# Kernel optimization log

Measured on AMD Instinct MI355X. Metric: run time of the kernel, lower is better.

## Reference

```python
import jax, jax.numpy as jnp
import numpy as np

MARGIN = 0.0  # init kwarg margin=0


def setup_inputs() -> dict:
    key = jax.random.key(0)
    k1, k2 = jax.random.split(key)
    inputs = jax.random.normal(k1, (4096, 2048), dtype=jnp.float32)
    targets = jax.random.randint(k2, (4096,), 0, 64, dtype=jnp.int64)
    return {"inputs": inputs, "targets": targets}


def _last_true_index(cond):
    # cond: (n, n) bool. Original torch loop zeros leading True entries until one
    # remains -> keeps the LAST True index per row.
    n = cond.shape[1]
    return (n - 1) - jnp.argmax(cond[:, ::-1], axis=1)


def reference(inputs, targets):
    n = inputs.shape[0]
    INF = jnp.asarray(jnp.inf, dtype=inputs.dtype)

    # pairwise euclidean distances: ||xi||^2 + ||xj||^2 - 2 xi.xj, clamp, sqrt
    sq = jnp.sum(inputs * inputs, axis=1)
    dist = sq[:, None] + sq[None, :] - 2.0 * (inputs @ inputs.T)
    dist = jnp.sqrt(jnp.clip(dist, 1e-12))  # (n, n)

    same = targets[:, None] == targets[None, :]  # (n, n) same-label mask

    # hardest positive / hardest negative per row
    dist_ap = jnp.where(same, dist, -INF).max(axis=1)
    dist_an = jnp.where(same, INF, dist).min(axis=1)

    # tie-broken indices (last occurrence, matching the torch loop)
    p = _last_true_index((dist == dist_ap[:, None]) & same)      # hardest pos idx
    q = _last_true_index((dist == dist_an[:, None]) & (~same))   # hardest neg idx

    # an2 = dist(hardest_pos_i, hardest_neg_i)
    dist_an2 = dist[p, q]

    # maskc: labels differing from both anchor's label and hardest-negative's label
    lbl_q = targets[q]
    maskc = (targets[None, :] != targets[:, None]) & (targets[None, :] != lbl_q[:, None])

    dist_q = dist[q]  # (n, n): distance rows of the hardest negatives
    ok_min = jnp.where(maskc, dist_q, INF).min(axis=1)
    r = _last_true_index((dist_q == ok_min[:, None]) & maskc)

    dist_an3 = dist[jnp.arange(n), r]  # dist(anchor, third-class sample)
    dist_an4 = dist_q[jnp.arange(n), r]  # dist(hardest neg, third-class sample) == ok_min

    # MarginRankingLoss(margin, reduce=False) with y=1: relu(ap - an + margin)
    loss = jax.nn.relu(dist_ap - dist_an + MARGIN)
    loss3 = jnp.abs(dist_an - dist_an2)
    loss4 = jnp.abs(dist_an3 - dist_an4)
    return (loss + loss3 + loss4).sum() / n
```

## Files before the change

### kernel.cpp

```cpp
#include <hip/hip_runtime.h>
#include <hip/hip_bf16.h>
#include <cstdint>

#define N_DIM 4096
#define K_DIM 2048
#define NKT 32
#define QSCALE 24.0f
#define QINV (1.0f / 24.0f)

typedef float floatx4 __attribute__((ext_vector_type(4)));
typedef int intx4 __attribute__((ext_vector_type(4)));
typedef unsigned short ushort8 __attribute__((ext_vector_type(8)));
typedef unsigned long long ull;

__device__ __forceinline__ unsigned short f2bf(float f) {
    unsigned int u = __builtin_bit_cast(unsigned int, f);
    unsigned int r = (u + 0x7fffu + ((u >> 16) & 1u)) >> 16;
    return (unsigned short)r;
}

__device__ __forceinline__ float bf2f(unsigned short b) {
    return __uint_as_float(((unsigned)b) << 16);
}

__device__ __forceinline__ void gld_lds16(const void* g, void* l) {
    __builtin_amdgcn_global_load_lds(
        (const __attribute__((address_space(1))) unsigned int*)g,
        (__attribute__((address_space(3))) unsigned int*)l,
        16, 0, 0);
}

__global__ __launch_bounds__(256)
void prep_kernel(const float* __restrict__ X, char* __restrict__ Qt,
                 int* __restrict__ sqi) {
    const int row = blockIdx.x;
    const int tid = threadIdx.x;
    const float* xr = X + (size_t)row * K_DIM;
    floatx4 a = *(const floatx4*)(xr + tid * 8);
    floatx4 b = *(const floatx4*)(xr + tid * 8 + 4);
    int s = 0;
    unsigned lo = 0, hi = 0;
#pragma unroll
    for (int e = 0; e < 4; ++e) {
        int v = __float2int_rn(a[e] * QSCALE);
        v = min(127, max(-127, v));
        s += v * v;
        lo |= ((unsigned)(v & 0xff)) << (8 * e);
        int w = __float2int_rn(b[e] * QSCALE);
        w = min(127, max(-127, w));
        s += w * w;
        hi |= ((unsigned)(w & 0xff)) << (8 * e);
    }
    *(int2*)(Qt + ((size_t)(tid >> 1) * 4096 + row) * 16 + (tid & 1) * 8) =
        make_int2((int)lo, (int)hi);
#pragma unroll
    for (int off = 32; off; off >>= 1) s += __shfl_down(s, off);
    __shared__ int wsum[4];
    const int wave = tid >> 6, lane = tid & 63;
    if (lane == 0) wsum[wave] = s;
    __syncthreads();
    if (tid == 0) sqi[row] = wsum[0] + wsum[1] + wsum[2] + wsum[3];
}

#define BAR() __builtin_amdgcn_s_barrier()
#define PRIO1() __builtin_amdgcn_s_setprio(1)
#define PRIO0() __builtin_amdgcn_s_setprio(0)
#define VMCNT3() asm volatile("s_waitcnt vmcnt(3)" ::: "memory")
#define VMCNT0() asm volatile("s_waitcnt vmcnt(0)" ::: "memory")
#define KTB 262144
#define STG(KT, BB) { \
    gld_lds16(aSt + (size_t)(KT) * KTB,          lds + (BB) + widB); \
    gld_lds16(aSt + (size_t)(KT) * KTB + 131072, lds + (BB) + 8192 + widB); \
    gld_lds16(bSt + (size_t)(KT) * KTB,          lds + (BB) + 16384 + widB); }

__global__ __launch_bounds__(512, 4)
void gemm_dist(const char* __restrict__ Qt, const int* __restrict__ sqi,
               unsigned short* __restrict__ Db) {
    __shared__ char lds[73728];
    const int tid = threadIdx.x;
    const int wid = tid >> 6, lane = tid & 63;
    const int wr = wid >> 1, wc = wid & 1;
    const int fr = lane & 15, ksub = lane >> 4;
    const int widB = wid * 1024;

    int rA[4], rB[4];
#pragma unroll
    for (int m = 0; m < 4; ++m) rA[m] = (ksub * 256 + wr * 64 + m * 16 + fr) * 16;
#pragma unroll
    for (int n = 0; n < 4; ++n) rB[n] = 16384 + (ksub * 128 + wc * 64 + n * 16 + fr) * 16;

    const int xcd = blockIdx.x & 7, kk = blockIdx.x >> 3;
    const int bi = (kk >> 3) | ((xcd & 1) << 3);
    const int bj = (kk & 7) | ((xcd >> 1) << 3);
    const int rowC0 = bi * 256, colC0 = bj * 128;

    const char* aSt = Qt + ((size_t)(tid >> 8) * 4096 + rowC0 + (tid & 255)) * 16;
    const char* bSt = Qt + ((size_t)(tid >> 7) * 4096 + colC0 + (tid & 127)) * 16;

    intx4 acc[4][4];
#pragma unroll
    for (int a1 = 0; a1 < 4; ++a1)
#pragma unroll
    for (int a2 = 0; a2 < 4; ++a2) acc[a1][a2] = (intx4){0, 0, 0, 0};
    intx4 af[4], bfv[4];

    STG(0, 0);
    STG(1, 24576);
    VMCNT3();
    BAR();

    int cb = 0, sb = 49152;
    for (int t = 0; t < NKT; ++t) {
        if (t < NKT - 2) STG(t + 2, sb);
#pragma unroll
        for (int m = 0; m < 4; ++m) af[m] = *(const intx4*)(lds + cb + rA[m]);
#pragma unroll
        for (int n = 0; n < 4; ++n) bfv[n] = *(const intx4*)(lds + cb + rB[n]);
        PRIO1();
#pragma unroll
        for (int n = 0; n < 4; ++n)
#pragma unroll
        for (int m = 0; m < 4; ++m)
            acc[n][m] = __builtin_amdgcn_mfma_i32_16x16x64_i8(
                af[m], bfv[n], acc[n][m], 0, 0, 0);
        PRIO0();
        if (t < NKT - 2) { VMCNT3(); } else if (t == NKT - 2) { VMCNT0(); }
        BAR();
        cb += 24576; if (cb >= 73728) cb = 0;
        sb += 24576; if (sb >= 73728) sb = 0;
    }

#pragma unroll
    for (int n = 0; n < 4; ++n) {
        const int col = colC0 + wc * 64 + n * 16 + fr;
        const int sqc = sqi[col];
#pragma unroll
        for (int m = 0; m < 4; ++m) {
            const int row0 = rowC0 + wr * 64 + m * 16 + ksub * 4;
#pragma unroll
            for (int r = 0; r < 4; ++r) {
                const int v = sqi[row0 + r] + sqc - 2 * acc[n][m][r];
                const float d = (v > 0) ? sqrtf((float)v) * QINV : 1e-6f;
                Db[(size_t)(row0 + r) * N_DIM + col] = f2bf(d);
            }
        }
    }
}

__global__ __launch_bounds__(256)
void stats_loss(const unsigned short* __restrict__ Db, const int* __restrict__ tgt,
                float* __restrict__ lossArr) {
    const int i = blockIdx.x, tid = threadIdx.x;
    const int ti = tgt[i];
    const unsigned short* row = Db + (size_t)i * N_DIM;
    ull kmax = 0ULL, kmin = ~0ULL;
#pragma unroll
    for (int it = 0; it < 2; ++it) {
        const int j0 = (it * 256 + tid) * 8;
        ushort8 d = *(const ushort8*)(row + j0);
        intx4 ta = *(const intx4*)(tgt + j0);
        intx4 tb = *(const intx4*)(tgt + j0 + 4);
#pragma unroll
        for (int e = 0; e < 8; ++e) {
            const int j = j0 + e;
            const int tl = (e < 4) ? ta[e] : tb[e - 4];
            const ull db = (ull)d[e] << 32;
            if (tl == ti) { ull k = db | (unsigned)j;  if (k > kmax) kmax = k; }
            else          { ull k = db | (unsigned)~j; if (k < kmin) kmin = k; }
        }
    }
    __shared__ ull sM[256], sN[256];
    sM[tid] = kmax; sN[tid] = kmin;
    __syncthreads();
    for (int off = 128; off; off >>= 1) {
        if (tid < off) {
            if (sM[tid + off] > sM[tid]) sM[tid] = sM[tid + off];
            if (sN[tid + off] < sN[tid]) sN[tid] = sN[tid + off];
        }
        __syncthreads();
    }
    const ull km = sM[0], kn = sN[0];
    const float ap = bf2f((unsigned short)(km >> 32));
    const int p = (int)(unsigned)(km & 0xFFFFFFFFu);
    const float an = bf2f((unsigned short)(kn >> 32));
    const int q = (int)~(unsigned)(kn & 0xFFFFFFFFu);
    __syncthreads();

    const int lq = tgt[q];
    const unsigned short* rowq = Db + (size_t)q * N_DIM;
    ull kr = ~0ULL;
#pragma unroll
    for (int it = 0; it < 2; ++it) {
        const int j0 = (it * 256 + tid) * 8;
        ushort8 d = *(const ushort8*)(rowq + j0);
        intx4 ta = *(const intx4*)(tgt + j0);
        intx4 tb = *(const intx4*)(tgt + j0 + 4);
#pragma unroll
        for (int e = 0; e < 8; ++e) {
            const int j = j0 + e;
            const int tl = (e < 4) ? ta[e] : tb[e - 4];
            if (tl != ti && tl != lq) {
                ull k = ((ull)d[e] << 32) | (unsigned)~j;
                if (k < kr) kr = k;
            }
        }
    }
    sN[tid] = kr;
    __syncthreads();
    for (int off = 128; off; off >>= 1) {
        if (tid < off) { if (sN[tid + off] < sN[tid]) sN[tid] = sN[tid + off]; }
        __syncthreads();
    }
    if (tid == 0) {
        const ull kk = sN[0];
        const float okmin = bf2f((unsigned short)(kk >> 32));
        const int r = (int)~(unsigned)(kk & 0xFFFFFFFFu);
        const float an2 = bf2f(Db[(size_t)p * N_DIM + q]);
        const float an3 = bf2f(Db[(size_t)i * N_DIM + r]);
        lossArr[i] = fmaxf(ap - an, 0.f) + fabsf(an - an2) + fabsf(an3 - okmin);
    }
}

__global__ __launch_bounds__(256)
void finred(const float* __restrict__ lossArr, float* __restrict__ out) {
    const int tid = threadIdx.x;
    float s = 0.f;
    for (int j = tid; j < N_DIM; j += 256) s += lossArr[j];
#pragma unroll
    for (int off = 32; off; off >>= 1) s += __shfl_down(s, off);
    __shared__ float w[4];
    const int wave = tid >> 6, lane = tid & 63;
    if (lane == 0) w[wave] = s;
    __syncthreads();
    if (tid == 0) out[0] = (w[0] + w[1] + w[2] + w[3]) * (1.0f / (float)N_DIM);
}

extern "C" void kernel_launch(void* const* d_in, const int* in_sizes, int n_in,
                              void* d_out, int out_size, void* d_ws, size_t ws_size,
                              hipStream_t stream) {
    const float* X = (const float*)d_in[0];
    const int* tgt = (const int*)d_in[1];
    float* out = (float*)d_out;

    char* w = (char*)d_ws;
    char* Qt = w;
    unsigned short* Db = (unsigned short*)(w + ((size_t)16 << 20));
    int* sqi = (int*)(w + ((size_t)80 << 20));
    float* lossArr = (float*)(sqi + N_DIM);

    prep_kernel<<<N_DIM, 256, 0, stream>>>(X, Qt, sqi);
    gemm_dist<<<512, 512, 0, stream>>>(Qt, sqi, Db);
    stats_loss<<<N_DIM, 256, 0, stream>>>(Db, tgt, lossArr);
    finred<<<1, 256, 0, stream>>>(lossArr, out);
}
```

Baseline: 78.61 us.

## Load A fragments directly into registers, stage only B through LDS

The A operand fragments now go straight from global memory into registers with inline-asm dwordx4 loads, double-buffered across two register sets. Only the B tile is still staged through LDS, using a smaller three-slot ring. This removes A's LDS write and read traffic and cuts LDS use from 72KB to 24KB per block. In exchange it raises register pressure, depends on hand-set vmcnt counts and sched_barriers for correctness, and uses less-coalesced global reads for A.

```diff
diff --git a/kernel.cpp b/kernel.cpp
--- a/kernel.cpp
+++ b/kernel.cpp
@@ -62,72 +62,75 @@
     if (tid == 0) sqi[row] = wsum[0] + wsum[1] + wsum[2] + wsum[3];
 }
 
-#define BAR() __builtin_amdgcn_s_barrier()
+#define BAR() { __builtin_amdgcn_s_barrier(); asm volatile("" ::: "memory"); }
 #define PRIO1() __builtin_amdgcn_s_setprio(1)
 #define PRIO0() __builtin_amdgcn_s_setprio(0)
-#define VMCNT3() asm volatile("s_waitcnt vmcnt(3)" ::: "memory")
-#define VMCNT0() asm volatile("s_waitcnt vmcnt(0)" ::: "memory")
+#define VMCNT5() { asm volatile("s_waitcnt vmcnt(5)" ::: "memory"); \
+                   __builtin_amdgcn_sched_barrier(0); }
+#define VMCNT0() { asm volatile("s_waitcnt vmcnt(0)" ::: "memory"); \
+                   __builtin_amdgcn_sched_barrier(0); }
 #define KTB 262144
-#define STG(KT, BB) { \
-    gld_lds16(aSt + (size_t)(KT) * KTB,          lds + (BB) + widB); \
-    gld_lds16(aSt + (size_t)(KT) * KTB + 131072, lds + (BB) + 8192 + widB); \
-    gld_lds16(bSt + (size_t)(KT) * KTB,          lds + (BB) + 16384 + widB); }
+#define LOAD_A(DST) { \
+    asm volatile("global_load_dwordx4 %0, %1, off"            : "=&v"(DST[0]) : "v"(aAddr)); \
+    asm volatile("global_load_dwordx4 %0, %1, off offset:256" : "=&v"(DST[1]) : "v"(aAddr)); \
+    asm volatile("global_load_dwordx4 %0, %1, off offset:512" : "=&v"(DST[2]) : "v"(aAddr)); \
+    asm volatile("global_load_dwordx4 %0, %1, off offset:768" : "=&v"(DST[3]) : "v"(aAddr)); \
+    aAddr += KTB; }
+#define MM16(AF) { _Pragma("unroll") for (int n_ = 0; n_ < 4; ++n_) { \
+    _Pragma("unroll") for (int m_ = 0; m_ < 4; ++m_) { \
+        acc[n_][m_] = __builtin_amdgcn_mfma_i32_16x16x64_i8( \
+            AF[m_], bfv[n_], acc[n_][m_], 0, 0, 0); } } }
+#define TILE_BODY(T, LD, USE) { \
+    if ((T) < NKT - 1) LOAD_A(LD); \
+    if ((T) < NKT - 1) { VMCNT5(); } else { VMCNT0(); } \
+    BAR(); \
+    if ((T) < NKT - 2) gld_lds16(bSrc + (size_t)((T) + 2) * KTB, lds + sb + widB); \
+    _Pragma("unroll") \
+    for (int n_ = 0; n_ < 4; ++n_) bfv[n_] = *(const intx4*)(lds + cb + rB[n_]); \
+    PRIO1(); MM16(USE); PRIO0(); \
+    cb += 8192; if (cb >= 24576) cb = 0; \
+    sb += 8192; if (sb >= 24576) sb = 0; }
 
 __global__ __launch_bounds__(512, 4)
 void gemm_dist(const char* __restrict__ Qt, const int* __restrict__ sqi,
                unsigned short* __restrict__ Db) {
-    __shared__ char lds[73728];
+    __shared__ char lds[24576];
     const int tid = threadIdx.x;
     const int wid = tid >> 6, lane = tid & 63;
     const int wr = wid >> 1, wc = wid & 1;
     const int fr = lane & 15, ksub = lane >> 4;
     const int widB = wid * 1024;
 
-    int rA[4], rB[4];
-#pragma unroll
-    for (int m = 0; m < 4; ++m) rA[m] = (ksub * 256 + wr * 64 + m * 16 + fr) * 16;
-#pragma unroll
-    for (int n = 0; n < 4; ++n) rB[n] = 16384 + (ksub * 128 + wc * 64 + n * 16 + fr) * 16;
+    int rB[4];
+#pragma unroll
+    for (int n = 0; n < 4; ++n) rB[n] = (ksub * 128 + wc * 64 + n * 16 + fr) * 16;
 
     const int xcd = blockIdx.x & 7, kk = blockIdx.x >> 3;
     const int bi = (kk >> 3) | ((xcd & 1) << 3);
     const int bj = (kk & 7) | ((xcd >> 1) << 3);
     const int rowC0 = bi * 256, colC0 = bj * 128;
 
-    const char* aSt = Qt + ((size_t)(tid >> 8) * 4096 + rowC0 + (tid & 255)) * 16;
-    const char* bSt = Qt + ((size_t)(tid >> 7) * 4096 + colC0 + (tid & 127)) * 16;
+    unsigned long long aAddr = (unsigned long long)(Qt +
+        ((size_t)ksub * 4096 + rowC0 + wr * 64 + fr) * 16);
+    const char* bSrc = Qt + ((size_t)(tid >> 7) * 4096 + colC0 + (tid & 127)) * 16;
 
     intx4 acc[4][4];
 #pragma unroll
     for (int a1 = 0; a1 < 4; ++a1)
 #pragma unroll
     for (int a2 = 0; a2 < 4; ++a2) acc[a1][a2] = (intx4){0, 0, 0, 0};
-    intx4 af[4], bfv[4];
-
-    STG(0, 0);
-    STG(1, 24576);
-    VMCNT3();
-    BAR();
-
-    int cb = 0, sb = 49152;
-    for (int t = 0; t < NKT; ++t) {
-        if (t < NKT - 2) STG(t + 2, sb);
-#pragma unroll
-        for (int m = 0; m < 4; ++m) af[m] = *(const intx4*)(lds + cb + rA[m]);
-#pragma unroll
-        for (int n = 0; n < 4; ++n) bfv[n] = *(const intx4*)(lds + cb + rB[n]);
-        PRIO1();
-#pragma unroll
-        for (int n = 0; n < 4; ++n)
-#pragma unroll
-        for (int m = 0; m < 4; ++m)
-            acc[n][m] = __builtin_amdgcn_mfma_i32_16x16x64_i8(
-                af[m], bfv[n], acc[n][m], 0, 0, 0);
-        PRIO0();
-        if (t < NKT - 2) { VMCNT3(); } else if (t == NKT - 2) { VMCNT0(); }
-        BAR();
-        cb += 24576; if (cb >= 73728) cb = 0;
-        sb += 24576; if (sb >= 73728) sb = 0;
+    intx4 afX[4], afY[4], bfv[4];
+
+    LOAD_A(afX);
+    gld_lds16(bSrc,       lds + 0    + widB);
+    gld_lds16(bSrc + KTB, lds + 8192 + widB);
+
+    int cb = 0, sb = 16384;
+#pragma unroll 1
+    for (int it = 0; it < NKT / 2; ++it) {
+        const int t0 = it * 2;
+        TILE_BODY(t0,     afY, afX);
+        TILE_BODY(t0 + 1, afX, afY);
     }
 
 #pragma unroll
```

Measured after the change: 78.90 us. No clear change (+0.4%).
